# Kernel optimization log

Hardware: AMD Instinct MI355X
Metric: run time of the kernel (lower is better)

## Reference

```python
import jax, jax.numpy as jnp
import numpy as np

NHEADS = 16
RANK = 8


def _rope(t):
    # t: (B, H, S, hd); past_len = 0 (no kv cache)
    hd = t.shape[-1]
    S = t.shape[2]
    inv = 1.0 / (10000.0 ** (jnp.arange(0, hd, 2, dtype=jnp.float32) / hd))  # (hd/2,)
    ang = jnp.arange(S, dtype=jnp.float32)[:, None] * inv[None, :]           # (S, hd/2)
    cos = jnp.concatenate([jnp.cos(ang), jnp.cos(ang)], -1)[None, None]      # (1,1,S,hd)
    sin = jnp.concatenate([jnp.sin(ang), jnp.sin(ang)], -1)[None, None]
    t1, t2 = jnp.split(t, 2, axis=-1)
    rot = jnp.concatenate([-t2, t1], -1)
    return t * cos + rot * sin


def _hyper_linear(x, Ws, bs, w1, b1, w2, b2, gA_w, gA_b, gB_w, gB_b):
    # Static path + per-batch dynamic low-rank correction generated from pooled context.
    B, S, D = x.shape
    z = x.mean(axis=1)                              # (B, D) pooled context
    h = jax.nn.silu(z @ w1 + b1)                    # (B, D/ratio)
    c = h @ w2 + b2                                 # (B, dynamic_dim)
    A = (c @ gA_w + gA_b).reshape(B, RANK, D)       # (B, rank, D_in)
    Bm = (c @ gB_w + gB_b).reshape(B, D, RANK)      # (B, D_out, rank)
    xa = jnp.einsum('bsd,brd->bsr', x, A)           # (B, S, rank)
    dyn = jnp.einsum('bsr,bor->bso', xa, Bm) / RANK # (B, S, D_out)
    return x @ Ws + bs + dyn


def _forward(x, Wq, bq, Wo, bo,
             Wk, bk, k_w1, k_b1, k_w2, k_b2, k_gA_w, k_gA_b, k_gB_w, k_gB_b,
             Wv, bv, v_w1, v_b1, v_w2, v_b2, v_gA_w, v_gA_b, v_gB_w, v_gB_b):
    B, S, D = x.shape
    hd = D // NHEADS
    q = x @ Wq + bq
    k = _hyper_linear(x, Wk, bk, k_w1, k_b1, k_w2, k_b2, k_gA_w, k_gA_b, k_gB_w, k_gB_b)
    v = _hyper_linear(x, Wv, bv, v_w1, v_b1, v_w2, v_b2, v_gA_w, v_gA_b, v_gB_w, v_gB_b)
    # (B, S, D) -> (B, H, S, hd)
    q = q.reshape(B, S, NHEADS, hd).transpose(0, 2, 1, 3)
    k = k.reshape(B, S, NHEADS, hd).transpose(0, 2, 1, 3)
    v = v.reshape(B, S, NHEADS, hd).transpose(0, 2, 1, 3)
    q = _rope(q)
    k = _rope(k)
    # causal SDPA (kv_cache is None -> is_causal=True)
    scale = 1.0 / jnp.sqrt(jnp.asarray(hd, dtype=x.dtype))
    scores = jnp.einsum('bhqd,bhkd->bhqk', q, k) * scale
    mask = jnp.tril(jnp.ones((S, S), dtype=bool))
    scores = jnp.where(mask, scores, jnp.asarray(-1e30, dtype=scores.dtype))
    attn = jax.nn.softmax(scores, axis=-1)
    out = jnp.einsum('bhqk,bhkd->bhqd', attn, v)
    out = out.transpose(0, 2, 1, 3).reshape(B, S, D)
    return out @ Wo + bo


def setup_inputs() -> dict:
    key = jax.random.key(0)
    D, HID, DYN = 1024, 256, 64
    B, S = 2, 2048
    ks = jax.random.split(key, 32)
    w = lambda i, shp: jax.random.normal(ks[i], shp, dtype=jnp.float32) * 0.02
    inp = {
        'x': jax.random.normal(ks[0], (B, S, D), dtype=jnp.float32),
        'Wq': w(1, (D, D)), 'bq': jnp.zeros((D,), jnp.float32),
        'Wo': w(2, (D, D)), 'bo': jnp.zeros((D,), jnp.float32),
        'Wk': w(3, (D, D)), 'bk': jnp.zeros((D,), jnp.float32),
        'k_w1': w(4, (D, HID)), 'k_b1': jnp.zeros((HID,), jnp.float32),
        'k_w2': w(5, (HID, DYN)), 'k_b2': jnp.zeros((DYN,), jnp.float32),
        'k_gA_w': w(6, (DYN, RANK * D)), 'k_gA_b': jnp.zeros((RANK * D,), jnp.float32),
        'k_gB_w': w(7, (DYN, D * RANK)), 'k_gB_b': jnp.zeros((D * RANK,), jnp.float32),
        'Wv': w(8, (D, D)), 'bv': jnp.zeros((D,), jnp.float32),
        'v_w1': w(9, (D, HID)), 'v_b1': jnp.zeros((HID,), jnp.float32),
        'v_w2': w(10, (HID, DYN)), 'v_b2': jnp.zeros((DYN,), jnp.float32),
        'v_gA_w': w(11, (DYN, RANK * D)), 'v_gA_b': jnp.zeros((RANK * D,), jnp.float32),
        'v_gB_w': w(12, (DYN, D * RANK)), 'v_gB_b': jnp.zeros((D * RANK,), jnp.float32),
    }
    return inp


def reference(x, Wq, bq, Wo, bo,
              Wk, bk, k_w1, k_b1, k_w2, k_b2, k_gA_w, k_gA_b, k_gB_w, k_gB_b,
              Wv, bv, v_w1, v_b1, v_w2, v_b2, v_gA_w, v_gA_b, v_gB_w, v_gB_b):
    return _forward(x, Wq, bq, Wo, bo,
                    Wk, bk, k_w1, k_b1, k_w2, k_b2, k_gA_w, k_gA_b, k_gB_w, k_gB_b,
                    Wv, bv, v_w1, v_b1, v_w2, v_b2, v_gA_w, v_gA_b, v_gB_w, v_gB_b)
```

## Files before the change

kernel.cpp:

```cpp
#include <hip/hip_runtime.h>
#include <math.h>

#define BB 2
#define SS 2048
#define DD 1024
#define NH 16
#define HDM 64
#define RNK 8

typedef short short8 __attribute__((ext_vector_type(8)));
typedef float floatx4 __attribute__((ext_vector_type(4)));

static __device__ __forceinline__ ushort f2bf(float f) {
  union { float f; unsigned u; } v;
  v.f = f;
  unsigned r = (v.u + 0x7FFFu + ((v.u >> 16) & 1u)) >> 16;
  return (ushort)r;
}
static __device__ __forceinline__ float bf2f(ushort u) {
  union { unsigned u; float f; } v;
  v.u = ((unsigned)u) << 16;
  return v.f;
}
static __device__ __forceinline__ unsigned pack_bf_trunc(float a, float b) {
  union { float f; unsigned u; } x, y;
  x.f = a;
  y.f = b;
  return __builtin_amdgcn_perm(y.u, x.u, 0x07060302u);
}
static __device__ __forceinline__ unsigned pack_bf_rne(float a, float b) {
  union { float f; unsigned u; } x, y;
  x.f = a;
  y.f = b;
  unsigned xu = x.u + 0x7FFFu + ((x.u >> 16) & 1u);
  unsigned yu = y.u + 0x7FFFu + ((y.u >> 16) & 1u);
  return __builtin_amdgcn_perm(yu, xu, 0x07060302u);
}

__global__ __launch_bounds__(256) void prep_all(
    const float* __restrict__ x, const float* __restrict__ Wq,
    const float* __restrict__ Wk, const float* __restrict__ Wv,
    const float* __restrict__ Wo, ushort* __restrict__ xb,
    ushort* __restrict__ Wcat, ushort* __restrict__ Wtk,
    ushort* __restrict__ Wtv, ushort* __restrict__ Wto,
    float2* __restrict__ tab, float* __restrict__ zsum) {
  __shared__ float tile[32][33];
  int blk = blockIdx.x;
  int tid = threadIdx.x;
  if (blk < 4096) {
    int gid = blk * 256 + tid;
    float4 a = ((const float4*)x)[gid];
    ushort4 o;
    o.x = f2bf(a.x);
    o.y = f2bf(a.y);
    o.z = f2bf(a.z);
    o.w = f2bf(a.w);
    ((ushort4*)xb)[gid] = o;
  } else if (blk < 8192) {
    int local = blk - 4096;
    int which = local >> 10;
    const float* W = which == 0 ? Wq : which == 1 ? Wk : which == 2 ? Wv : Wo;
    ushort* Wt = which == 0 ? Wcat : which == 1 ? Wtk : which == 2 ? Wtv : Wto;
    int t = local & 1023;
    int bx = t & 31, by = t >> 5;
    int tx = tid & 31, ty = tid >> 5;
#pragma unroll
    for (int i = 0; i < 4; ++i)
      tile[ty + 8 * i][tx] =
          W[(size_t)(by * 32 + ty + 8 * i) * DD + bx * 32 + tx];
    __syncthreads();
#pragma unroll
    for (int i = 0; i < 4; ++i)
      Wt[(size_t)(bx * 32 + ty + 8 * i) * DD + by * 32 + tx] =
          f2bf(tile[tx][ty + 8 * i]);
  } else if (blk < 8448) {
    int gid = (blk - 8192) * 256 + tid;
    int i = gid >> 11, s = gid & 2047;
    float freq = expf(-(float)i * (9.210340371976184f / 32.0f));
    float sn, cn;
    sincosf((float)s * freq, &sn, &cn);
    tab[gid] = make_float2(cn, sn);
  } else {
    int lb = blk - 8448;
    int b = lb >> 7;
    int s0 = (lb & 127) * 16;
    float p0 = 0.f, p1 = 0.f, p2 = 0.f, p3 = 0.f;
    const float* xp = x + ((size_t)b * SS + s0) * DD;
    for (int s = 0; s < 16; ++s) {
      const float* row = xp + (size_t)s * DD;
      p0 += row[tid];
      p1 += row[tid + 256];
      p2 += row[tid + 512];
      p3 += row[tid + 768];
    }
    atomicAdd(&zsum[b * DD + tid], p0);
    atomicAdd(&zsum[b * DD + tid + 256], p1);
    atomicAdd(&zsum[b * DD + tid + 512], p2);
    atomicAdd(&zsum[b * DD + tid + 768], p3);
  }
}

__global__ __launch_bounds__(256) void gen_h(
    const float* __restrict__ zsum,
    const float* __restrict__ kw1, const float* __restrict__ vw1,
    float* __restrict__ h_pre) {
  int b = blockIdx.x & 1;
  int p = (blockIdx.x >> 1) & 1;
  int slice = blockIdx.y;
  const float* w1 = p ? vw1 : kw1;
  int tid = threadIdx.x;
  float acc = 0.f;
  int j0 = slice * 128;
  for (int j = j0; j < j0 + 128; ++j) {
    float z = zsum[b * DD + j] * (1.0f / (float)SS);
    acc += z * w1[j * 256 + tid];
  }
  atomicAdd(&h_pre[(p * 2 + b) * 256 + tid], acc);
}

__global__ __launch_bounds__(256) void hyper_c2(
    const float* __restrict__ h_pre,
    const float* __restrict__ kb1, const float* __restrict__ kw2,
    const float* __restrict__ kb2,
    const float* __restrict__ vb1, const float* __restrict__ vw2,
    const float* __restrict__ vb2, float* __restrict__ c_all) {
  int p = blockIdx.x >> 1;
  int b = blockIdx.x & 1;
  const float* b1 = p ? vb1 : kb1;
  const float* w2 = p ? vw2 : kw2;
  const float* b2 = p ? vb2 : kb2;
  __shared__ float hs[256];
  __shared__ float part[256];
  int tid = threadIdx.x;
  float hv = h_pre[(p * 2 + b) * 256 + tid] + b1[tid];
  hs[tid] = hv / (1.0f + expf(-hv));
  __syncthreads();
  int n = tid & 63, chunk = tid >> 6;
  float a = 0.f;
  for (int jj = 0; jj < 64; ++jj) {
    int j = chunk * 64 + jj;
    a += hs[j] * w2[j * 64 + n];
  }
  part[tid] = a;
  __syncthreads();
  if (tid < 64) {
    c_all[(p * 2 + b) * 64 + tid] =
        part[tid] + part[tid + 64] + part[tid + 128] + part[tid + 192] + b2[tid];
  }
}

__global__ __launch_bounds__(256) void gen_AB(
    const float* __restrict__ c_all,
    const float* __restrict__ kgAw, const float* __restrict__ kgAb,
    const float* __restrict__ kgBw, const float* __restrict__ kgBb,
    const float* __restrict__ vgAw, const float* __restrict__ vgAb,
    const float* __restrict__ vgBw, const float* __restrict__ vgBb,
    float* __restrict__ Ak, float* __restrict__ Bk,
    float* __restrict__ Av, float* __restrict__ Bv) {
  int y = blockIdx.y;
  int p = y >> 1, mat = y & 1;
  const float* gw = p ? (mat ? vgBw : vgAw) : (mat ? kgBw : kgAw);
  const float* gb = p ? (mat ? vgBb : vgAb) : (mat ? kgBb : kgAb);
  float* obase = p ? (mat ? Bv : Av) : (mat ? Bk : Ak);

  __shared__ float c0[64], c1[64];
  int tid = threadIdx.x;
  if (tid < 64) c0[tid] = c_all[p * 128 + tid];
  else if (tid < 128) c1[tid - 64] = c_all[p * 128 + tid];
  __syncthreads();

  int idx = blockIdx.x * 256 + tid;
  float a0 = gb[idx], a1 = a0;
#pragma unroll
  for (int j = 0; j < 64; ++j) {
    float w = gw[j * (RNK * DD) + idx];
    a0 += c0[j] * w;
    a1 += c1[j] * w;
  }
  obase[idx] = a0;
  obase[RNK * DD + idx] = a1;
}

__global__ __launch_bounds__(256) void weff(
    const float* __restrict__ Ak, const float* __restrict__ Bk,
    const float* __restrict__ Av, const float* __restrict__ Bv,
    const ushort* __restrict__ Wtk, const ushort* __restrict__ Wtv,
    ushort* __restrict__ Wcat) {
  int y = blockIdx.y;
  int p = y >> 1, b = y & 1;
  const float* A = (p ? Av : Ak) + b * (RNK * DD);
  const float* Bm = (p ? Bv : Bk) + b * (RNK * DD);
  const ushort* src = p ? Wtv : Wtk;
  ushort* dst = Wcat + ((size_t)(1 + 2 * p + b) << 20);

  int tid = threadIdx.x;
  int row = blockIdx.x * 16 + (tid >> 4);
  int cg = tid & 15;
  float bm[RNK];
#pragma unroll
  for (int r = 0; r < RNK; ++r) bm[r] = Bm[row * RNK + r];
  for (int kk = cg * 64; kk < cg * 64 + 64; kk += 4) {
    float4 acc = make_float4(0.f, 0.f, 0.f, 0.f);
#pragma unroll
    for (int r = 0; r < RNK; ++r) {
      float4 a4 = *(const float4*)&A[r * DD + kk];
      acc.x += bm[r] * a4.x;
      acc.y += bm[r] * a4.y;
      acc.z += bm[r] * a4.z;
      acc.w += bm[r] * a4.w;
    }
    ushort4 ws = *(const ushort4*)&src[(size_t)row * DD + kk];
    ushort4 o;
    o.x = f2bf(bf2f(ws.x) + acc.x * 0.125f);
    o.y = f2bf(bf2f(ws.y) + acc.y * 0.125f);
    o.z = f2bf(bf2f(ws.z) + acc.z * 0.125f);
    o.w = f2bf(bf2f(ws.w) + acc.w * 0.125f);
    *(ushort4*)&dst[(size_t)row * DD + kk] = o;
  }
}

__global__ __launch_bounds__(256) void gemm_qkv(
    const ushort* __restrict__ Axb, const ushort* __restrict__ Wcat,
    const float* __restrict__ bq, const float* __restrict__ bk,
    const float* __restrict__ bv, const float2* __restrict__ tab,
    ushort* __restrict__ qhb, ushort* __restrict__ khb,
    ushort* __restrict__ vhb) {
  __shared__ ushort As[128][40];
  __shared__ ushort Bs[128][40];
  int tid = threadIdx.x;
  int bm = blockIdx.x * 128;
  int ny = blockIdx.y;
  int path = ny >> 3;
  int nb = (ny & 7) * 128;
  int b_blk = bm >> 11;
  const ushort* Wbase =
      (path == 0) ? Wcat : Wcat + ((size_t)(1 + (path - 1) * 2 + b_blk) << 20);
  const float* bias = (path == 0) ? bq : (path == 1 ? bk : bv);
  ushort* outp = (path == 0) ? qhb : (path == 1 ? khb : vhb);

  int w = tid >> 6, lane = tid & 63, l16 = lane & 15, q4 = lane >> 4;
  int wm = (w >> 1) * 64, wn = (w & 1) * 64;
  floatx4 acc[4][4];
#pragma unroll
  for (int mi = 0; mi < 4; ++mi)
#pragma unroll
    for (int ni = 0; ni < 4; ++ni) acc[mi][ni] = 0;

  int sr = tid >> 2, sc = (tid & 3) * 8;
  const ushort* Ap0 = Axb + (size_t)(bm + sr) * DD + sc;
  const ushort* Ap1 = Axb + (size_t)(bm + sr + 64) * DD + sc;
  const ushort* Bp0 = Wbase + (size_t)(nb + sr) * DD + sc;
  const ushort* Bp1 = Wbase + (size_t)(nb + sr + 64) * DD + sc;

  for (int k0 = 0; k0 < DD; k0 += 32) {
    uint4 a0 = *(const uint4*)(Ap0 + k0);
    uint4 a1 = *(const uint4*)(Ap1 + k0);
    uint4 b0 = *(const uint4*)(Bp0 + k0);
    uint4 b1 = *(const uint4*)(Bp1 + k0);
    __syncthreads();
    *(uint4*)&As[sr][sc] = a0;
    *(uint4*)&As[sr + 64][sc] = a1;
    *(uint4*)&Bs[sr][sc] = b0;
    *(uint4*)&Bs[sr + 64][sc] = b1;
    __syncthreads();
    short8 af[4], bf[4];
#pragma unroll
    for (int mi = 0; mi < 4; ++mi)
      af[mi] = *(const short8*)&As[wm + mi * 16 + l16][q4 * 8];
#pragma unroll
    for (int ni = 0; ni < 4; ++ni)
      bf[ni] = *(const short8*)&Bs[wn + ni * 16 + l16][q4 * 8];
#pragma unroll
    for (int mi = 0; mi < 4; ++mi)
#pragma unroll
      for (int ni = 0; ni < 4; ++ni)
        acc[mi][ni] = __builtin_amdgcn_mfma_f32_16x16x32_bf16(
            af[mi], bf[ni], acc[mi][ni], 0, 0, 0);
  }

  int h = (nb + wn) >> 6;
  float biasv[4];
#pragma unroll
  for (int ni = 0; ni < 4; ++ni) biasv[ni] = bias[nb + wn + ni * 16 + l16];

#pragma unroll
  for (int mi = 0; mi < 4; ++mi) {
#pragma unroll
    for (int r = 0; r < 4; ++r) {
      int grow = bm + wm + mi * 16 + q4 * 4 + r;
      int bb = grow >> 11, s = grow & 2047;
      ushort* orow = outp + (((size_t)(bb * NH + h) * SS + s) << 6);
      float v[4];
#pragma unroll
      for (int ni = 0; ni < 4; ++ni) v[ni] = acc[mi][ni][r] + biasv[ni];
      if (path < 2) {
#pragma unroll
        for (int ni = 0; ni < 2; ++ni) {
          float2 cs = tab[((ni * 16 + l16) << 11) + s];
          float a = v[ni] * cs.x - v[ni + 2] * cs.y;
          float c = v[ni + 2] * cs.x + v[ni] * cs.y;
          v[ni] = a;
          v[ni + 2] = c;
        }
      }
#pragma unroll
      for (int ni = 0; ni < 4; ++ni) orow[ni * 16 + l16] = f2bf(v[ni]);
    }
  }
}

#define VT_IDX(d, c) ((unsigned)(72 * (d) + 16 * ((d) >> 3) + (c)))

__global__ __launch_bounds__(128) void attn_mfma3(
    const ushort* __restrict__ qh, const ushort* __restrict__ kh,
    const ushort* __restrict__ vh, ushort* __restrict__ ao) {
  __shared__ ushort Ps[64][72];
  __shared__ ushort Vt[2][4720];
  int bid = blockIdx.x;
  int bh = bid & 31;
  int q0 = (31 - (bid >> 5)) * 64;
  int b = bh >> 4, h = bh & 15;
  int tid = threadIdx.x;
  int w = tid >> 6, lane = tid & 63, l16 = lane & 15, q4 = lane >> 4;
  int nkt = (q0 >> 6) + 1;

  const ushort* kbase = kh + (size_t)bh * SS * HDM;
  const ushort* vbase = vh + (size_t)bh * SS * HDM;

  short8 qf[2][2];
#pragma unroll
  for (int qi = 0; qi < 2; ++qi) {
    const ushort* qrow = qh + ((size_t)bh * SS + q0 + 32 * w + 16 * qi + l16) * HDM;
    qf[qi][0] = *(const short8*)(qrow + 8 * q4);
    qf[qi][1] = *(const short8*)(qrow + 32 + 8 * q4);
  }

  int so8 = tid & 7, sp = (tid >> 3) & 15;

  short8 kf[4][2];
#pragma unroll
  for (int ki = 0; ki < 4; ++ki) {
    const ushort* kr = kbase + (size_t)(16 * ki + l16) * HDM + 8 * q4;
    kf[ki][0] = *(const short8*)(kr);
    kf[ki][1] = *(const short8*)(kr + 32);
  }
  uint4 vr[4];
#pragma unroll
  for (int j = 0; j < 4; ++j)
    vr[j] = *(const uint4*)(vbase + (size_t)(4 * sp + j) * HDM + 8 * so8);
#pragma unroll
  for (int j = 0; j < 4; j += 2) {
    const ushort* pa = (const ushort*)&vr[j];
    const ushort* pb = (const ushort*)&vr[j + 1];
#pragma unroll
    for (int dd = 0; dd < 8; ++dd) {
      int d = so8 * 8 + dd;
      *(unsigned*)&Vt[0][VT_IDX(d, 4 * sp + j)] =
          (unsigned)pa[dd] | ((unsigned)pb[dd] << 16);
    }
  }
  __syncthreads();

  floatx4 o[4][2];
#pragma unroll
  for (int di = 0; di < 4; ++di)
#pragma unroll
    for (int qi = 0; qi < 2; ++qi) o[di][qi] = 0;
  float l_part[2] = {0.f, 0.f};

  for (int kt = 0; kt < nkt; ++kt) {
    int buf = kt & 1;
    bool has_next = (kt + 1) < nkt;
    short8 kn[4][2];
    if (has_next) {
      int k0n = (kt + 1) * 64;
#pragma unroll
      for (int ki = 0; ki < 4; ++ki) {
        const ushort* kr = kbase + (size_t)(k0n + 16 * ki + l16) * HDM + 8 * q4;
        kn[ki][0] = *(const short8*)(kr);
        kn[ki][1] = *(const short8*)(kr + 32);
      }
#pragma unroll
      for (int j = 0; j < 4; ++j)
        vr[j] = *(const uint4*)(vbase + (size_t)(k0n + 4 * sp + j) * HDM + 8 * so8);
    }

    floatx4 s4[2][4];
#pragma unroll
    for (int ki = 0; ki < 4; ++ki)
#pragma unroll
      for (int qi = 0; qi < 2; ++qi) {
        floatx4 c;
        c = 0;
        c = __builtin_amdgcn_mfma_f32_16x16x32_bf16(kf[ki][0], qf[qi][0], c, 0, 0, 0);
        c = __builtin_amdgcn_mfma_f32_16x16x32_bf16(kf[ki][1], qf[qi][1], c, 0, 0, 0);
        s4[qi][ki] = c;
      }

    bool diag = (kt == nkt - 1);
#pragma unroll
    for (int qi = 0; qi < 2; ++qi) {
      int qloc = 32 * w + 16 * qi + l16;
      float lp = 0.f;
#pragma unroll
      for (int ki = 0; ki < 4; ++ki) {
        float p[4];
#pragma unroll
        for (int r = 0; r < 4; ++r) {
          float t = s4[qi][ki][r] * 0.18033688f;
          float pv = exp2f(t);
          if (diag && (16 * ki + 4 * q4 + r) > qloc) pv = 0.f;
          p[r] = pv;
          lp += pv;
        }
        uint2 u2;
        u2.x = pack_bf_trunc(p[0], p[1]);
        u2.y = pack_bf_trunc(p[2], p[3]);
        *(uint2*)&Ps[qloc][16 * ki + 4 * q4] = u2;
      }
      l_part[qi] += lp;
    }

#pragma unroll
    for (int qi = 0; qi < 2; ++qi) {
      short8 pf0 = *(const short8*)&Ps[32 * w + 16 * qi + l16][8 * q4];
      short8 pf1 = *(const short8*)&Ps[32 * w + 16 * qi + l16][32 + 8 * q4];
#pragma unroll
      for (int di = 0; di < 4; ++di) {
        short8 vf0 = *(const short8*)&Vt[buf][VT_IDX(16 * di + l16, 8 * q4)];
        short8 vf1 = *(const short8*)&Vt[buf][VT_IDX(16 * di + l16, 32 + 8 * q4)];
        o[di][qi] =
            __builtin_amdgcn_mfma_f32_16x16x32_bf16(vf0, pf0, o[di][qi], 0, 0, 0);
        o[di][qi] =
            __builtin_amdgcn_mfma_f32_16x16x32_bf16(vf1, pf1, o[di][qi], 0, 0, 0);
      }
    }

    if (has_next) {
      int nb = (kt + 1) & 1;
#pragma unroll
      for (int j = 0; j < 4; j += 2) {
        const ushort* pa = (const ushort*)&vr[j];
        const ushort* pb = (const ushort*)&vr[j + 1];
#pragma unroll
        for (int dd = 0; dd < 8; ++dd) {
          int d = so8 * 8 + dd;
          *(unsigned*)&Vt[nb][VT_IDX(d, 4 * sp + j)] =
              (unsigned)pa[dd] | ((unsigned)pb[dd] << 16);
        }
      }
#pragma unroll
      for (int ki = 0; ki < 4; ++ki) {
        kf[ki][0] = kn[ki][0];
        kf[ki][1] = kn[ki][1];
      }
    }
    __syncthreads();
  }

#pragma unroll
  for (int qi = 0; qi < 2; ++qi) {
    float l = l_part[qi];
    l += __shfl_xor(l, 16);
    l += __shfl_xor(l, 32);
    float inv = 1.0f / l;
    int token = q0 + 32 * w + 16 * qi + l16;
    ushort* orow = ao + ((size_t)(b * SS + token)) * DD + h * HDM;
#pragma unroll
    for (int di = 0; di < 4; ++di) {
      floatx4 ov = o[di][qi];
      uint2 u2;
      u2.x = pack_bf_rne(ov[0] * inv, ov[1] * inv);
      u2.y = pack_bf_rne(ov[2] * inv, ov[3] * inv);
      *(uint2*)&orow[16 * di + 4 * q4] = u2;
    }
  }
}

__global__ __launch_bounds__(256) void gemm_out(
    const ushort* __restrict__ A, const ushort* __restrict__ Bt,
    const float* __restrict__ bias, float* __restrict__ C) {
  __shared__ ushort As[64][40];
  __shared__ ushort Bs[128][40];
  int tid = threadIdx.x;
  int bm = blockIdx.x * 64, bn = blockIdx.y * 128;
  int w = tid >> 6, lane = tid & 63, l16 = lane & 15, q4 = lane >> 4;
  int wm = (w >> 1) * 32, wn = (w & 1) * 64;
  floatx4 acc[2][4];
#pragma unroll
  for (int mi = 0; mi < 2; ++mi)
#pragma unroll
    for (int ni = 0; ni < 4; ++ni) acc[mi][ni] = 0;

  int sr = tid >> 2, sc = (tid & 3) * 8;
  const ushort* Ap0 = A + (size_t)(bm + sr) * DD + sc;
  const ushort* Bp0 = Bt + (size_t)(bn + sr) * DD + sc;
  const ushort* Bp1 = Bt + (size_t)(bn + sr + 64) * DD + sc;

  for (int k0 = 0; k0 < DD; k0 += 32) {
    uint4 a0 = *(const uint4*)(Ap0 + k0);
    uint4 b0 = *(const uint4*)(Bp0 + k0);
    uint4 b1 = *(const uint4*)(Bp1 + k0);
    __syncthreads();
    *(uint4*)&As[sr & 63][sc] = a0;
    *(uint4*)&Bs[sr][sc] = b0;
    *(uint4*)&Bs[sr + 64][sc] = b1;
    __syncthreads();
    short8 af[2], bf[4];
#pragma unroll
    for (int mi = 0; mi < 2; ++mi)
      af[mi] = *(const short8*)&As[wm + mi * 16 + l16][q4 * 8];
#pragma unroll
    for (int ni = 0; ni < 4; ++ni)
      bf[ni] = *(const short8*)&Bs[wn + ni * 16 + l16][q4 * 8];
#pragma unroll
    for (int mi = 0; mi < 2; ++mi)
#pragma unroll
      for (int ni = 0; ni < 4; ++ni)
        acc[mi][ni] = __builtin_amdgcn_mfma_f32_16x16x32_bf16(
            af[mi], bf[ni], acc[mi][ni], 0, 0, 0);
  }
#pragma unroll
  for (int mi = 0; mi < 2; ++mi) {
#pragma unroll
    for (int r = 0; r < 4; ++r) {
      int row = bm + wm + mi * 16 + q4 * 4 + r;
      float* Cr = C + (size_t)row * DD;
#pragma unroll
      for (int ni = 0; ni < 4; ++ni) {
        int col = bn + wn + ni * 16 + l16;
        Cr[col] = acc[mi][ni][r] + bias[col];
      }
    }
  }
}

extern "C" void kernel_launch(void* const* d_in, const int* in_sizes, int n_in,
                              void* d_out, int out_size, void* d_ws,
                              size_t ws_size, hipStream_t stream) {
  const float* x    = (const float*)d_in[0];
  const float* Wq   = (const float*)d_in[1];
  const float* bq   = (const float*)d_in[2];
  const float* Wo   = (const float*)d_in[3];
  const float* bo   = (const float*)d_in[4];
  const float* Wk   = (const float*)d_in[5];
  const float* bk   = (const float*)d_in[6];
  const float* kw1  = (const float*)d_in[7];
  const float* kb1  = (const float*)d_in[8];
  const float* kw2  = (const float*)d_in[9];
  const float* kb2  = (const float*)d_in[10];
  const float* kgAw = (const float*)d_in[11];
  const float* kgAb = (const float*)d_in[12];
  const float* kgBw = (const float*)d_in[13];
  const float* kgBb = (const float*)d_in[14];
  const float* Wv   = (const float*)d_in[15];
  const float* bv   = (const float*)d_in[16];
  const float* vw1  = (const float*)d_in[17];
  const float* vb1  = (const float*)d_in[18];
  const float* vw2  = (const float*)d_in[19];
  const float* vb2  = (const float*)d_in[20];
  const float* vgAw = (const float*)d_in[21];
  const float* vgAb = (const float*)d_in[22];
  const float* vgBw = (const float*)d_in[23];
  const float* vgBb = (const float*)d_in[24];
  float* out = (float*)d_out;

  char* ws = (char*)d_ws;
  const size_t MB = 1024 * 1024;
  ushort* qhb  = (ushort*)(ws);
  ushort* khb  = (ushort*)(ws + 8 * MB);
  ushort* vhb  = (ushort*)(ws + 16 * MB);
  ushort* xb   = (ushort*)(ws + 24 * MB);
  ushort* aob  = (ushort*)(ws + 32 * MB);
  ushort* Wcat = (ushort*)(ws + 40 * MB);
  ushort* Wto  = (ushort*)(ws + 50 * MB);
  ushort* Wtk  = (ushort*)(ws + 52 * MB);
  ushort* Wtv  = (ushort*)(ws + 54 * MB);
  float*  Ak   = (float*)(ws + 56 * MB);
  float*  Bk   = Ak + BB * RNK * DD;
  float*  Av   = Bk + BB * RNK * DD;
  float*  Bv   = Av + BB * RNK * DD;
  float*  zsum = Bv + BB * RNK * DD;
  float*  h_pre = zsum + BB * DD;
  float*  c_all = h_pre + 4 * 256;
  float2* tab  = (float2*)(ws + 56 * MB + 512 * 1024);

  hipMemsetAsync(zsum, 0, (BB * DD + 4 * 256) * sizeof(float), stream);
  prep_all<<<8704, 256, 0, stream>>>(x, Wq, Wk, Wv, Wo, xb, Wcat, Wtk, Wtv,
                                     Wto, tab, zsum);
  gen_h<<<dim3(4, 8), 256, 0, stream>>>(zsum, kw1, vw1, h_pre);
  hyper_c2<<<4, 256, 0, stream>>>(h_pre, kb1, kw2, kb2, vb1, vw2, vb2, c_all);
  gen_AB<<<dim3(RNK * DD / 256, 4), 256, 0, stream>>>(
      c_all, kgAw, kgAb, kgBw, kgBb, vgAw, vgAb, vgBw, vgBb, Ak, Bk, Av, Bv);
  weff<<<dim3(64, 4), 256, 0, stream>>>(Ak, Bk, Av, Bv, Wtk, Wtv, Wcat);

  gemm_qkv<<<dim3(32, 24), 256, 0, stream>>>(xb, Wcat, bq, bk, bv, tab, qhb,
                                             khb, vhb);
  attn_mfma3<<<1024, 128, 0, stream>>>(qhb, khb, vhb, aob);
  gemm_out<<<dim3(64, 8), 256, 0, stream>>>(aob, Wto, bo, out);
}
```

Baseline: 313.5 us.

## Split causal attention along the KV axis with atomic partial accumulation and a normalize pass

Long query tiles are now split into chunks of up to eight KV tiles. The work goes to 2560 blocks instead of 1024, which evens out the causal load imbalance. Split blocks add unnormalized outputs and row sums into fp32 global buffers with atomics, and a new normalize kernel converts those rows to bf16. The softmax has no running max, so partial sums can be added directly. The change costs a 17MB memset, many scattered float atomics (strided, uncoalesced), and an extra kernel launch.

```diff
diff --git a/kernel.cpp b/kernel.cpp
--- a/kernel.cpp
+++ b/kernel.cpp
@@ -311,18 +311,40 @@
 
 #define VT_IDX(d, c) ((unsigned)(72 * (d) + 16 * ((d) >> 3) + (c)))
 
-__global__ __launch_bounds__(128) void attn_mfma3(
+__global__ __launch_bounds__(128) void attn_split(
     const ushort* __restrict__ qh, const ushort* __restrict__ kh,
-    const ushort* __restrict__ vh, ushort* __restrict__ ao) {
+    const ushort* __restrict__ vh, ushort* __restrict__ ao,
+    float* __restrict__ Oacc, float* __restrict__ Lacc) {
   __shared__ ushort Ps[64][72];
   __shared__ ushort Vt[2][4720];
   int bid = blockIdx.x;
   int bh = bid & 31;
-  int q0 = (31 - (bid >> 5)) * 64;
+  int tt = 79 - (bid >> 5);
+  int s, c;
+  if (tt < 8) {
+    s = tt;
+    c = 0;
+  } else if (tt < 24) {
+    int u = tt - 8;
+    s = 8 + (u >> 1);
+    c = u & 1;
+  } else if (tt < 48) {
+    int u = tt - 24;
+    int d3 = u / 3;
+    s = 16 + d3;
+    c = u - 3 * d3;
+  } else {
+    int u = tt - 48;
+    s = 24 + (u >> 2);
+    c = u & 3;
+  }
+  int q0 = s * 64;
+  int kt0 = c * 8;
+  int kend = kt0 + 8;
+  if (kend > s + 1) kend = s + 1;
   int b = bh >> 4, h = bh & 15;
   int tid = threadIdx.x;
   int w = tid >> 6, lane = tid & 63, l16 = lane & 15, q4 = lane >> 4;
-  int nkt = (q0 >> 6) + 1;
 
   const ushort* kbase = kh + (size_t)bh * SS * HDM;
   const ushort* vbase = vh + (size_t)bh * SS * HDM;
@@ -330,7 +352,8 @@
   short8 qf[2][2];
 #pragma unroll
   for (int qi = 0; qi < 2; ++qi) {
-    const ushort* qrow = qh + ((size_t)bh * SS + q0 + 32 * w + 16 * qi + l16) * HDM;
+    const ushort* qrow =
+        qh + ((size_t)bh * SS + q0 + 32 * w + 16 * qi + l16) * HDM;
     qf[qi][0] = *(const short8*)(qrow + 8 * q4);
     qf[qi][1] = *(const short8*)(qrow + 32 + 8 * q4);
   }
@@ -340,14 +363,15 @@
   short8 kf[4][2];
 #pragma unroll
   for (int ki = 0; ki < 4; ++ki) {
-    const ushort* kr = kbase + (size_t)(16 * ki + l16) * HDM + 8 * q4;
+    const ushort* kr = kbase + (size_t)(kt0 * 64 + 16 * ki + l16) * HDM + 8 * q4;
     kf[ki][0] = *(const short8*)(kr);
     kf[ki][1] = *(const short8*)(kr + 32);
   }
   uint4 vr[4];
 #pragma unroll
   for (int j = 0; j < 4; ++j)
-    vr[j] = *(const uint4*)(vbase + (size_t)(4 * sp + j) * HDM + 8 * so8);
+    vr[j] =
+        *(const uint4*)(vbase + (size_t)(kt0 * 64 + 4 * sp + j) * HDM + 8 * so8);
 #pragma unroll
   for (int j = 0; j < 4; j += 2) {
     const ushort* pa = (const ushort*)&vr[j];
@@ -368,9 +392,9 @@
     for (int qi = 0; qi < 2; ++qi) o[di][qi] = 0;
   float l_part[2] = {0.f, 0.f};
 
-  for (int kt = 0; kt < nkt; ++kt) {
-    int buf = kt & 1;
-    bool has_next = (kt + 1) < nkt;
+  for (int kt = kt0; kt < kend; ++kt) {
+    int buf = (kt - kt0) & 1;
+    bool has_next = (kt + 1) < kend;
     short8 kn[4][2];
     if (has_next) {
       int k0n = (kt + 1) * 64;
@@ -382,7 +406,8 @@
       }
 #pragma unroll
       for (int j = 0; j < 4; ++j)
-        vr[j] = *(const uint4*)(vbase + (size_t)(k0n + 4 * sp + j) * HDM + 8 * so8);
+        vr[j] =
+            *(const uint4*)(vbase + (size_t)(k0n + 4 * sp + j) * HDM + 8 * so8);
     }
 
     floatx4 s4[2][4];
@@ -390,14 +415,16 @@
     for (int ki = 0; ki < 4; ++ki)
 #pragma unroll
       for (int qi = 0; qi < 2; ++qi) {
-        floatx4 c;
-        c = 0;
-        c = __builtin_amdgcn_mfma_f32_16x16x32_bf16(kf[ki][0], qf[qi][0], c, 0, 0, 0);
-        c = __builtin_amdgcn_mfma_f32_16x16x32_bf16(kf[ki][1], qf[qi][1], c, 0, 0, 0);
-        s4[qi][ki] = c;
-      }
-
-    bool diag = (kt == nkt - 1);
+        floatx4 cc;
+        cc = 0;
+        cc = __builtin_amdgcn_mfma_f32_16x16x32_bf16(kf[ki][0], qf[qi][0], cc,
+                                                     0, 0, 0);
+        cc = __builtin_amdgcn_mfma_f32_16x16x32_bf16(kf[ki][1], qf[qi][1], cc,
+                                                     0, 0, 0);
+        s4[qi][ki] = cc;
+      }
+
+    bool diag = (kt == s);
 #pragma unroll
     for (int qi = 0; qi < 2; ++qi) {
       int qloc = 32 * w + 16 * qi + l16;
@@ -428,7 +455,8 @@
 #pragma unroll
       for (int di = 0; di < 4; ++di) {
         short8 vf0 = *(const short8*)&Vt[buf][VT_IDX(16 * di + l16, 8 * q4)];
-        short8 vf1 = *(const short8*)&Vt[buf][VT_IDX(16 * di + l16, 32 + 8 * q4)];
+        short8 vf1 =
+            *(const short8*)&Vt[buf][VT_IDX(16 * di + l16, 32 + 8 * q4)];
         o[di][qi] =
             __builtin_amdgcn_mfma_f32_16x16x32_bf16(vf0, pf0, o[di][qi], 0, 0, 0);
         o[di][qi] =
@@ -437,7 +465,7 @@
     }
 
     if (has_next) {
-      int nb = (kt + 1) & 1;
+      int nb = (kt + 1 - kt0) & 1;
 #pragma unroll
       for (int j = 0; j < 4; j += 2) {
         const ushort* pa = (const ushort*)&vr[j];
@@ -463,17 +491,84 @@
     float l = l_part[qi];
     l += __shfl_xor(l, 16);
     l += __shfl_xor(l, 32);
-    float inv = 1.0f / l;
-    int token = q0 + 32 * w + 16 * qi + l16;
-    ushort* orow = ao + ((size_t)(b * SS + token)) * DD + h * HDM;
-#pragma unroll
-    for (int di = 0; di < 4; ++di) {
-      floatx4 ov = o[di][qi];
-      uint2 u2;
-      u2.x = pack_bf_rne(ov[0] * inv, ov[1] * inv);
-      u2.y = pack_bf_rne(ov[2] * inv, ov[3] * inv);
-      *(uint2*)&orow[16 * di + 4 * q4] = u2;
-    }
+    l_part[qi] = l;
+  }
+
+  if (s < 8) {
+#pragma unroll
+    for (int qi = 0; qi < 2; ++qi) {
+      float inv = 1.0f / l_part[qi];
+      int token = q0 + 32 * w + 16 * qi + l16;
+      ushort* orow = ao + ((size_t)(b * SS + token)) * DD + h * HDM;
+#pragma unroll
+      for (int di = 0; di < 4; ++di) {
+        floatx4 ov = o[di][qi];
+        uint2 u2;
+        u2.x = pack_bf_rne(ov[0] * inv, ov[1] * inv);
+        u2.y = pack_bf_rne(ov[2] * inv, ov[3] * inv);
+        *(uint2*)&orow[16 * di + 4 * q4] = u2;
+      }
+    }
+  } else {
+    float* Ob = Oacc + (size_t)bh * 64 * SS;
+#pragma unroll
+    for (int qi = 0; qi < 2; ++qi) {
+      int token = q0 + 32 * w + 16 * qi + l16;
+      if (q4 == 0) atomicAdd(&Lacc[bh * SS + token], l_part[qi]);
+#pragma unroll
+      for (int di = 0; di < 4; ++di) {
+#pragma unroll
+        for (int r = 0; r < 4; ++r)
+          atomicAdd(&Ob[(size_t)(16 * di + 4 * q4 + r) * SS + token],
+                    o[di][qi][r]);
+      }
+    }
+  }
+}
+
+__global__ __launch_bounds__(256) void attn_norm(
+    const float* __restrict__ Oacc, const float* __restrict__ Lacc,
+    ushort* __restrict__ ao) {
+  __shared__ float tile[64][129];
+  int bh = blockIdx.y;
+  int s0 = (blockIdx.x + 4) * 128;
+  int b = bh >> 4, h = bh & 15;
+  int tid = threadIdx.x;
+  const float* Ob = Oacc + (size_t)bh * 64 * SS;
+#pragma unroll
+  for (int i = 0; i < 32; ++i) {
+    int idx = i * 256 + tid;
+    int d = idx >> 7, tok = idx & 127;
+    tile[d][tok] = Ob[(size_t)d * SS + s0 + tok];
+  }
+  __syncthreads();
+#pragma unroll
+  for (int i = 0; i < 2; ++i) {
+    int u = i * 256 + tid;
+    int tok = u >> 2, qtr = u & 3;
+    float inv = 1.0f / Lacc[bh * SS + s0 + tok];
+    ushort* orow = ao + ((size_t)(b * SS + s0 + tok)) * DD + h * HDM + qtr * 16;
+    uint2 u2a, u2b;
+    u2a.x = pack_bf_rne(tile[qtr * 16 + 0][tok] * inv,
+                        tile[qtr * 16 + 1][tok] * inv);
+    u2a.y = pack_bf_rne(tile[qtr * 16 + 2][tok] * inv,
+                        tile[qtr * 16 + 3][tok] * inv);
+    *(uint2*)&orow[0] = u2a;
+    u2a.x = pack_bf_rne(tile[qtr * 16 + 4][tok] * inv,
+                        tile[qtr * 16 + 5][tok] * inv);
+    u2a.y = pack_bf_rne(tile[qtr * 16 + 6][tok] * inv,
+                        tile[qtr * 16 + 7][tok] * inv);
+    *(uint2*)&orow[4] = u2a;
+    u2b.x = pack_bf_rne(tile[qtr * 16 + 8][tok] * inv,
+                        tile[qtr * 16 + 9][tok] * inv);
+    u2b.y = pack_bf_rne(tile[qtr * 16 + 10][tok] * inv,
+                        tile[qtr * 16 + 11][tok] * inv);
+    *(uint2*)&orow[8] = u2b;
+    u2b.x = pack_bf_rne(tile[qtr * 16 + 12][tok] * inv,
+                        tile[qtr * 16 + 13][tok] * inv);
+    u2b.y = pack_bf_rne(tile[qtr * 16 + 14][tok] * inv,
+                        tile[qtr * 16 + 15][tok] * inv);
+    *(uint2*)&orow[12] = u2b;
   }
 }
 
@@ -571,9 +666,9 @@
   ushort* khb  = (ushort*)(ws + 8 * MB);
   ushort* vhb  = (ushort*)(ws + 16 * MB);
   ushort* xb   = (ushort*)(ws + 24 * MB);
-  ushort* aob  = (ushort*)(ws + 32 * MB);
-  ushort* Wcat = (ushort*)(ws + 40 * MB);
-  ushort* Wto  = (ushort*)(ws + 50 * MB);
+  ushort* Wto  = (ushort*)(ws + 32 * MB);
+  ushort* aob2 = (ushort*)(ws + 34 * MB);
+  ushort* Wcat = (ushort*)(ws + 42 * MB);
   ushort* Wtk  = (ushort*)(ws + 52 * MB);
   ushort* Wtv  = (ushort*)(ws + 54 * MB);
   float*  Ak   = (float*)(ws + 56 * MB);
@@ -584,6 +679,9 @@
   float*  h_pre = zsum + BB * DD;
   float*  c_all = h_pre + 4 * 256;
   float2* tab  = (float2*)(ws + 56 * MB + 512 * 1024);
+  size_t ooff = (ws_size - 17 * MB) & ~(size_t)255;
+  float* Oacc = (float*)(ws + ooff);
+  float* Lacc = (float*)(ws + ooff + 16 * MB);
 
   hipMemsetAsync(zsum, 0, (BB * DD + 4 * 256) * sizeof(float), stream);
   prep_all<<<8704, 256, 0, stream>>>(x, Wq, Wk, Wv, Wo, xb, Wcat, Wtk, Wtv,
@@ -596,6 +694,9 @@
 
   gemm_qkv<<<dim3(32, 24), 256, 0, stream>>>(xb, Wcat, bq, bk, bv, tab, qhb,
                                              khb, vhb);
-  attn_mfma3<<<1024, 128, 0, stream>>>(qhb, khb, vhb, aob);
-  gemm_out<<<dim3(64, 8), 256, 0, stream>>>(aob, Wto, bo, out);
-}
+  hipMemsetAsync(Oacc, 0, 16 * MB + (size_t)BB * NH * SS * sizeof(float),
+                 stream);
+  attn_split<<<2560, 128, 0, stream>>>(qhb, khb, vhb, aob2, Oacc, Lacc);
+  attn_norm<<<dim3(12, 32), 256, 0, stream>>>(Oacc, Lacc, aob2);
+  gemm_out<<<dim3(64, 8), 256, 0, stream>>>(aob2, Wto, bo, out);
+}
```

Result: slower. 348.1 us (+11.0%).
